# Kernel optimization log

Measured on AMD Instinct MI355X. Metric: run time of the kernel, lower is better.

## Reference

```python
import jax, jax.numpy as jnp
import numpy as np

PI = np.pi
EPS_A = 1e-4


def _frft_1d(x, a):
    """Chirp-z shear FRFT along the last axis. x: complex (..., N), a: scalar order."""
    a = jnp.clip(a, EPS_A, 2.0 - EPS_A)
    N = x.shape[-1]
    x = jnp.fft.ifftshift(x, axes=-1)
    alpha = a * PI / 2.0
    tan_a2 = jnp.tan(a * PI / 4.0)
    sin_a = jnp.sin(alpha)
    n = (jnp.arange(N, dtype=jnp.float32) - (N // 2))  # [-N/2, N/2)
    c1 = jnp.exp(-1j * PI * (n ** 2) * tan_a2 / N)      # chirp (depends on a)
    c2 = jnp.exp(-1j * PI * (n ** 2) / (N * sin_a))     # kernel chirp
    y = jnp.fft.ifft(jnp.fft.fft(x * c1, axis=-1) * c2, axis=-1)
    y = y * c1 / jnp.sqrt(jnp.abs(sin_a) + 1e-12)
    return jnp.fft.fftshift(y, axes=-1)


def _frft2d(x, ax, ay):
    # width pass (last axis) with ay, then height pass with ax -- same math as the
    # per-row / per-column torch loops, fully batched.
    y = _frft_1d(x, ay)                                   # over W
    y = jnp.swapaxes(_frft_1d(jnp.swapaxes(y, -1, -2), ax), -1, -2)  # over H
    return y


def setup_inputs() -> dict:
    key = jax.random.key(0)
    kx, = jax.random.split(key, 1)
    B, C, H, W = 4, 32, 256, 256
    x = jax.random.normal(kx, (B, C, H, W), dtype=jnp.float32)
    alpha = jnp.float32(0.5)
    # 1x1 conv weight (C, 2C): module init = copy of magnitude channels
    w = jnp.zeros((C, 2 * C), dtype=jnp.float32)
    w = w.at[jnp.arange(C), jnp.arange(C)].set(1.0)
    return {"x": x, "alpha": alpha, "w": w}


def reference(x, alpha, w):
    Xc = x.astype(jnp.complex64)
    Y = _frft2d(Xc, alpha, alpha)                        # (B, C, H, W) complex
    out = jnp.concatenate([jnp.abs(Y), jnp.angle(Y) / PI], axis=1)  # (B, 2C, H, W)
    out = jnp.einsum('oc,bchw->bohw', w, out)            # 1x1 conv, no bias
    return out.astype(x.dtype)
```

## Files before the change

kernel.cpp:

```cpp
#include <hip/hip_runtime.h>
#include <math.h>

#define B_N 4
#define C_N 32
#define H_N 256
#define W_N 256
#define PI_D 3.14159265358979323846
#define LSQ 257
#define LDW 260

typedef _Float16 half8 __attribute__((ext_vector_type(8)));
typedef float f32x4 __attribute__((ext_vector_type(4)));

__device__ __forceinline__ float2 cmul(float2 a, float2 b) {
    return make_float2(a.x * b.x - a.y * b.y, a.x * b.y + a.y * b.x);
}
__device__ __forceinline__ float2 f2add(float2 a, float2 b) {
    return make_float2(a.x + b.x, a.y + b.y);
}
__device__ __forceinline__ float2 f2sub(float2 a, float2 b) {
    return make_float2(a.x - b.x, a.y - b.y);
}

__device__ __forceinline__ void make_tables(int tid, const float* __restrict__ alpha_p,
                                            float2* c1l, float2* c2l, float2* twl,
                                            float* sscl) {
    if (tid < 256) {
        int j = tid;
        double a = fmin(fmax((double)alpha_p[0], 1e-4), 2.0 - 1e-4);
        double tan_a2 = tan(a * PI_D / 4.0);
        double sin_a  = sin(a * PI_D / 2.0);
        double n = (double)(j - 128);
        float sn, cs;

        double u1 = n * n * tan_a2 * (1.0 / 256.0);
        u1 -= 2.0 * floor(u1 * 0.5);
        __sincosf((float)(-PI_D * u1), &sn, &cs);
        c1l[j] = make_float2(cs, sn);

        double u2 = n * n / (256.0 * sin_a);
        u2 -= 2.0 * floor(u2 * 0.5);
        __sincosf((float)(-PI_D * u2), &sn, &cs);
        c2l[j] = make_float2(cs, sn);

        int k1 = j >> 4, t = j & 15;
        __sincosf((float)(-2.0 * PI_D * (double)(t * k1) * (1.0 / 256.0)), &sn, &cs);
        twl[j] = make_float2(cs, sn);

        if (j == 0) *sscl = (float)(1.0 / sqrt(fabs(sin_a) + 1e-12));
    }
}

template <bool INV>
__device__ __forceinline__ void fft16(float2* v) {
    const float C1 = 0.9238795325112867f, S1 = 0.3826834323650898f;
    const float C2 = 0.7071067811865476f;
    const float2 tw1 = make_float2(C1, INV ? S1 : -S1);
    const float2 tw2 = make_float2(C2, INV ? C2 : -C2);
    const float2 tw3 = make_float2(S1, INV ? C1 : -C1);
    const float2 tw4 = make_float2(0.0f, INV ? 1.0f : -1.0f);
    const float2 tw6 = make_float2(-C2, INV ? C2 : -C2);
    const float2 tw9 = make_float2(-C1, INV ? -S1 : S1);
    float2 u[16];
    #pragma unroll
    for (int n2 = 0; n2 < 4; ++n2) {
        float2 e0 = v[n2], e1 = v[4 + n2], e2 = v[8 + n2], e3 = v[12 + n2];
        float2 t0 = f2add(e0, e2), t1 = f2sub(e0, e2);
        float2 t2 = f2add(e1, e3), t3 = f2sub(e1, e3);
        float2 A0 = f2add(t0, t2);
        float2 A2 = f2sub(t0, t2);
        float2 A1, A3;
        if (!INV) { A1 = make_float2(t1.x + t3.y, t1.y - t3.x);
                    A3 = make_float2(t1.x - t3.y, t1.y + t3.x); }
        else      { A1 = make_float2(t1.x - t3.y, t1.y + t3.x);
                    A3 = make_float2(t1.x + t3.y, t1.y - t3.x); }
        u[n2] = A0;
        if (n2 == 0) { u[4 + n2] = A1;            u[8 + n2] = A2;            u[12 + n2] = A3; }
        if (n2 == 1) { u[4 + n2] = cmul(A1, tw1); u[8 + n2] = cmul(A2, tw2); u[12 + n2] = cmul(A3, tw3); }
        if (n2 == 2) { u[4 + n2] = cmul(A1, tw2); u[8 + n2] = cmul(A2, tw4); u[12 + n2] = cmul(A3, tw6); }
        if (n2 == 3) { u[4 + n2] = cmul(A1, tw3); u[8 + n2] = cmul(A2, tw6); u[12 + n2] = cmul(A3, tw9); }
    }
    #pragma unroll
    for (int k1 = 0; k1 < 4; ++k1) {
        float2 e0 = u[4 * k1], e1 = u[4 * k1 + 1], e2 = u[4 * k1 + 2], e3 = u[4 * k1 + 3];
        float2 t0 = f2add(e0, e2), t1 = f2sub(e0, e2);
        float2 t2 = f2add(e1, e3), t3 = f2sub(e1, e3);
        v[4 * k1 + 0] = f2add(t0, t2);
        v[4 * k1 + 2] = f2sub(t0, t2);
        if (!INV) { v[4 * k1 + 1] = make_float2(t1.x + t3.y, t1.y - t3.x);
                    v[4 * k1 + 3] = make_float2(t1.x - t3.y, t1.y + t3.x); }
        else      { v[4 * k1 + 1] = make_float2(t1.x - t3.y, t1.y + t3.x);
                    v[4 * k1 + 3] = make_float2(t1.x + t3.y, t1.y - t3.x); }
    }
}
#define REG(k) (4 * ((k) & 3) + ((k) >> 2))

__device__ __forceinline__ void frft_core16(float2* v, float2* __restrict__ sp,
                                            int t,
                                            const float2* __restrict__ c2l,
                                            const float2* __restrict__ twl) {
    fft16<false>(v);
    float2 w[16];
    #pragma unroll
    for (int k1 = 0; k1 < 16; ++k1)
        w[k1] = cmul(v[REG(k1)], twl[16 * k1 + t]);
    #pragma unroll
    for (int k1 = 0; k1 < 16; ++k1)
        sp[16 * k1 + (t ^ k1)] = w[k1];
    __syncthreads();
    #pragma unroll
    for (int n2 = 0; n2 < 16; ++n2)
        v[n2] = sp[16 * t + (n2 ^ t)];
    fft16<false>(v);
    #pragma unroll
    for (int k2 = 0; k2 < 16; ++k2)
        w[k2] = cmul(v[REG(k2)], c2l[t + 16 * k2]);
    fft16<true>(w);
    __syncthreads();
    #pragma unroll
    for (int m2 = 0; m2 < 16; ++m2) {
        float2 tw = twl[16 * m2 + t];
        tw.y = -tw.y;
        sp[16 * m2 + (t ^ m2)] = cmul(w[REG(m2)], tw);
    }
    __syncthreads();
    #pragma unroll
    for (int k1 = 0; k1 < 16; ++k1)
        v[k1] = sp[16 * t + (k1 ^ t)];
    fft16<true>(v);
}

__global__ __launch_bounds__(512, 4) void frft_cols_real(
        const float* __restrict__ x,
        const float* __restrict__ alpha_p,
        float2* __restrict__ Y) {
    __shared__ float2 s[32 * LSQ];
    __shared__ float2 c1l[256], c2l[256], twl[256];
    __shared__ float sscl;
    int tid = threadIdx.x;

    int blk = blockIdx.x;
    int w0 = (blk & 7) << 5;
    long long bc = blk >> 3;
    const float* xb = x + (bc << 16) + w0;

    float4 xv[4];
    #pragma unroll
    for (int p = 0; p < 4; ++p) {
        int idx = tid + (p << 9);
        int row = idx >> 3, c4 = idx & 7;
        xv[p] = *(const float4*)(xb + row * W_N + (c4 << 2));
    }

    make_tables(tid, alpha_p, c1l, c2l, twl, &sscl);

    float* fs = (float*)s;
    #pragma unroll
    for (int p = 0; p < 4; ++p) {
        int idx = tid + (p << 9);
        int row = idx >> 3, c4 = idx & 7;
        fs[(4 * c4 + 0) * (2 * LSQ) + row] = xv[p].x;
        fs[(4 * c4 + 1) * (2 * LSQ) + row] = xv[p].y;
        fs[(4 * c4 + 2) * (2 * LSQ) + row] = xv[p].z;
        fs[(4 * c4 + 3) * (2 * LSQ) + row] = xv[p].w;
    }
    __syncthreads();

    int seq = tid & 31, t = tid >> 5;
    float xs[16];
    #pragma unroll
    for (int n1 = 0; n1 < 16; ++n1)
        xs[n1] = fs[seq * (2 * LSQ) + 16 * (n1 ^ 8) + t];
    float scl_v = sscl;
    __syncthreads();

    float2 v[16];
    #pragma unroll
    for (int n1 = 0; n1 < 16; ++n1) {
        float2 c = c1l[16 * n1 + t];
        v[n1] = make_float2(xs[n1] * c.x, xs[n1] * c.y);
    }

    frft_core16(v, s + seq * LSQ, t, c2l, twl);

    float sc = scl_v * (1.0f / 256.0f);
    float2* Yb = Y + (bc << 16) + w0 + seq;
    #pragma unroll
    for (int m1 = 0; m1 < 16; ++m1) {
        float2 o = cmul(v[REG(m1)], c1l[16 * m1 + t]);
        Yb[(16 * (m1 ^ 8) + t) * W_N] = make_float2(o.x * sc, o.y * sc);
    }
}

__device__ __forceinline__ float fast_atan2(float y, float x) {
    float ax = fabsf(x), ay = fabsf(y);
    float mx = fmaxf(ax, ay), mn = fminf(ax, ay);
    float z = mn * __builtin_amdgcn_rcpf(fmaxf(mx, 1e-37f));
    float z2 = z * z;
    float p = fmaf(z2, -0.01172120f, 0.05265332f);
    p = fmaf(z2, p, -0.11643287f);
    p = fmaf(z2, p, 0.19354346f);
    p = fmaf(z2, p, -0.33262347f);
    p = fmaf(z2, p, 0.99997726f);
    p = p * z;
    float r = (ay > ax) ? (1.5707963f - p) : p;
    r = (x < 0.0f) ? (3.14159265f - r) : r;
    return copysignf(r, y);
}

__global__ __launch_bounds__(512, 4) void frft_rows_conv(
        const float2* __restrict__ Y,
        const float* __restrict__ alpha_p,
        const float* __restrict__ wmat, float* __restrict__ out) {
    __shared__ float2 s[32 * LSQ];
    __shared__ float2 c1l[256], c2l[256], twl[256];
    __shared__ float sscl;
    int tid = threadIdx.x;
    int t = tid & 15, ch = tid >> 4;

    int b = blockIdx.x >> 8, h = blockIdx.x & 255;
    const float2* xr = Y + (((long long)(b * C_N + ch)) << 16) + (h << 8);

    float2 v[16];
    #pragma unroll
    for (int n1 = 0; n1 < 16; ++n1)
        v[n1] = xr[16 * (n1 ^ 8) + t];

    make_tables(tid, alpha_p, c1l, c2l, twl, &sscl);
    __syncthreads();

    #pragma unroll
    for (int n1 = 0; n1 < 16; ++n1)
        v[n1] = cmul(v[n1], c1l[16 * n1 + t]);

    float2* sp = s + ch * LSQ;
    frft_core16(v, sp, t, c2l, twl);

    float sc = sscl * (1.0f / 256.0f);
    #pragma unroll
    for (int m1 = 0; m1 < 16; ++m1) {
        float2 o = cmul(v[REG(m1)], c1l[16 * m1 + t]);
        float mg = sc * sqrtf(fmaf(o.x, o.x, o.y * o.y));
        float an = fast_atan2(o.y, o.x) * 0.31830988618f;
        sp[16 * (m1 ^ 8) + t] = make_float2(mg, an);
    }
    __syncthreads();

    int lane = tid & 63, wv = tid >> 6;
    int q = lane >> 4, l15 = lane & 15;

    half8 bf[2][2];
    #pragma unroll
    for (int nt = 0; nt < 2; ++nt)
        #pragma unroll
        for (int kt = 0; kt < 2; ++kt) {
            const float* wp = wmat + (nt * 16 + l15) * 64 + kt * 32 + q * 8;
            float4 wa = *(const float4*)wp;
            float4 wb = *(const float4*)(wp + 4);
            bf[nt][kt][0] = (_Float16)wa.x; bf[nt][kt][1] = (_Float16)wa.y;
            bf[nt][kt][2] = (_Float16)wa.z; bf[nt][kt][3] = (_Float16)wa.w;
            bf[nt][kt][4] = (_Float16)wb.x; bf[nt][kt][5] = (_Float16)wb.y;
            bf[nt][kt][6] = (_Float16)wb.z; bf[nt][kt][7] = (_Float16)wb.w;
        }

    f32x4 acc[2][2];
    #pragma unroll
    for (int i = 0; i < 2; ++i)
        #pragma unroll
        for (int j = 0; j < 2; ++j)
            acc[i][j] = (f32x4){0.0f, 0.0f, 0.0f, 0.0f};

    #pragma unroll
    for (int mt2 = 0; mt2 < 2; ++mt2) {
        int mt = wv * 2 + mt2;
        int w = mt * 16 + l15;
        half8 am, aa;
        #pragma unroll
        for (int j = 0; j < 8; ++j) {
            float2 fv = s[(q * 8 + j) * LSQ + w];
            am[j] = (_Float16)fv.x;
            aa[j] = (_Float16)fv.y;
        }
        #pragma unroll
        for (int nt = 0; nt < 2; ++nt) {
            acc[mt2][nt] = __builtin_amdgcn_mfma_f32_16x16x32_f16(am, bf[nt][0], acc[mt2][nt], 0, 0, 0);
            acc[mt2][nt] = __builtin_amdgcn_mfma_f32_16x16x32_f16(aa, bf[nt][1], acc[mt2][nt], 0, 0, 0);
        }
    }
    __syncthreads();

    float* Ob = (float*)s;
    #pragma unroll
    for (int mt2 = 0; mt2 < 2; ++mt2) {
        int mt = wv * 2 + mt2;
        #pragma unroll
        for (int nt = 0; nt < 2; ++nt) {
            int o = nt * 16 + l15;
            *(f32x4*)&Ob[o * LDW + mt * 16 + q * 4] = acc[mt2][nt];
        }
    }
    __syncthreads();

    int o2 = tid >> 4, i16 = tid & 15;
    float* ob = out + (((long long)(b * C_N + o2)) << 16) + (h << 8);
    #pragma unroll
    for (int p = 0; p < 4; ++p) {
        int w4 = i16 * 4 + (p << 6);
        f32x4 val = *(f32x4*)&Ob[o2 * LDW + w4];
        *(f32x4*)(ob + w4) = val;
    }
}

extern "C" void kernel_launch(void* const* d_in, const int* in_sizes, int n_in,
                              void* d_out, int out_size, void* d_ws, size_t ws_size,
                              hipStream_t stream) {
    const float* x     = (const float*)d_in[0];
    const float* alpha = (const float*)d_in[1];
    const float* wmat  = (const float*)d_in[2];
    float* out = (float*)d_out;

    float2* Y = (float2*)d_ws;

    frft_cols_real<<<B_N * C_N * (W_N / 32), 512, 0, stream>>>(x, alpha, Y);

    frft_rows_conv<<<B_N * H_N, 512, 0, stream>>>(Y, alpha, wmat, out);
}
```

Baseline: 128.6 us.

## Make FFTs wave-local, stage column output in LDS, replace MFMA conv with FMA

The thread-to-sequence mapping in the column kernel becomes 16 threads per sequence, so each FFT lives inside one wavefront and the block-wide barriers in the FFT core become wave barriers. The column kernel now stages its output through LDS and writes Y as coalesced 16-byte rows instead of strided float2 stores. The row kernel's MFMA half-precision 1x1 conv, with its LDS transpose, is replaced by a per-thread fp32 FMA loop that reads weights with uniform scalar loads, and the launch-bounds occupancy hints are dropped. The conv now runs in fp32 on vector ALUs rather than matrix cores, and the weight reads and output stores are laid out differently.

```diff
diff --git a/kernel.cpp b/kernel.cpp
--- a/kernel.cpp
+++ b/kernel.cpp
@@ -7,9 +7,8 @@
 #define W_N 256
 #define PI_D 3.14159265358979323846
 #define LSQ 257
-#define LDW 260
-
-typedef _Float16 half8 __attribute__((ext_vector_type(8)));
+#define YROW 34
+
 typedef float f32x4 __attribute__((ext_vector_type(4)));
 
 __device__ __forceinline__ float2 cmul(float2 a, float2 b) {
@@ -107,7 +106,7 @@
     #pragma unroll
     for (int k1 = 0; k1 < 16; ++k1)
         sp[16 * k1 + (t ^ k1)] = w[k1];
-    __syncthreads();
+    __builtin_amdgcn_wave_barrier();
     #pragma unroll
     for (int n2 = 0; n2 < 16; ++n2)
         v[n2] = sp[16 * t + (n2 ^ t)];
@@ -116,25 +115,25 @@
     for (int k2 = 0; k2 < 16; ++k2)
         w[k2] = cmul(v[REG(k2)], c2l[t + 16 * k2]);
     fft16<true>(w);
-    __syncthreads();
+    __builtin_amdgcn_wave_barrier();
     #pragma unroll
     for (int m2 = 0; m2 < 16; ++m2) {
         float2 tw = twl[16 * m2 + t];
         tw.y = -tw.y;
         sp[16 * m2 + (t ^ m2)] = cmul(w[REG(m2)], tw);
     }
-    __syncthreads();
+    __builtin_amdgcn_wave_barrier();
     #pragma unroll
     for (int k1 = 0; k1 < 16; ++k1)
         v[k1] = sp[16 * t + (k1 ^ t)];
     fft16<true>(v);
 }
 
-__global__ __launch_bounds__(512, 4) void frft_cols_real(
+__global__ __launch_bounds__(512) void frft_cols_real(
         const float* __restrict__ x,
         const float* __restrict__ alpha_p,
         float2* __restrict__ Y) {
-    __shared__ float2 s[32 * LSQ];
+    __shared__ float2 s[H_N * YROW];
     __shared__ float2 c1l[256], c2l[256], twl[256];
     __shared__ float sscl;
     int tid = threadIdx.x;
@@ -166,13 +165,13 @@
     }
     __syncthreads();
 
-    int seq = tid & 31, t = tid >> 5;
+    int t = tid & 15, seq = tid >> 4;
     float xs[16];
     #pragma unroll
     for (int n1 = 0; n1 < 16; ++n1)
         xs[n1] = fs[seq * (2 * LSQ) + 16 * (n1 ^ 8) + t];
     float scl_v = sscl;
-    __syncthreads();
+    __builtin_amdgcn_wave_barrier();
 
     float2 v[16];
     #pragma unroll
@@ -184,11 +183,26 @@
     frft_core16(v, s + seq * LSQ, t, c2l, twl);
 
     float sc = scl_v * (1.0f / 256.0f);
-    float2* Yb = Y + (bc << 16) + w0 + seq;
+    float2 ov[16];
     #pragma unroll
     for (int m1 = 0; m1 < 16; ++m1) {
         float2 o = cmul(v[REG(m1)], c1l[16 * m1 + t]);
-        Yb[(16 * (m1 ^ 8) + t) * W_N] = make_float2(o.x * sc, o.y * sc);
+        ov[m1] = make_float2(o.x * sc, o.y * sc);
+    }
+    __syncthreads();
+
+    #pragma unroll
+    for (int m1 = 0; m1 < 16; ++m1)
+        s[(16 * (m1 ^ 8) + t) * YROW + seq] = ov[m1];
+    __syncthreads();
+
+    int seq2 = tid & 15, rr = tid >> 4;
+    float2* Yb = Y + (bc << 16) + w0;
+    #pragma unroll
+    for (int p = 0; p < 8; ++p) {
+        int row = rr + (p << 5);
+        f32x4 val = *(f32x4*)&s[row * YROW + 2 * seq2];
+        *(f32x4*)(Yb + (long long)row * W_N + 2 * seq2) = val;
     }
 }
 
@@ -208,7 +222,7 @@
     return copysignf(r, y);
 }
 
-__global__ __launch_bounds__(512, 4) void frft_rows_conv(
+__global__ __launch_bounds__(512) void frft_rows_conv(
         const float2* __restrict__ Y,
         const float* __restrict__ alpha_p,
         const float* __restrict__ wmat, float* __restrict__ out) {
@@ -237,6 +251,7 @@
     frft_core16(v, sp, t, c2l, twl);
 
     float sc = sscl * (1.0f / 256.0f);
+    __builtin_amdgcn_wave_barrier();
     #pragma unroll
     for (int m1 = 0; m1 < 16; ++m1) {
         float2 o = cmul(v[REG(m1)], c1l[16 * m1 + t]);
@@ -246,69 +261,28 @@
     }
     __syncthreads();
 
-    int lane = tid & 63, wv = tid >> 6;
-    int q = lane >> 4, l15 = lane & 15;
-
-    half8 bf[2][2];
-    #pragma unroll
-    for (int nt = 0; nt < 2; ++nt)
+    int w = tid & 255;
+    int obase = __builtin_amdgcn_readfirstlane((tid >> 8) << 4);
+    const float* wrow = wmat + obase * 64;
+
+    float acc[16];
+    #pragma unroll
+    for (int o = 0; o < 16; ++o) acc[o] = 0.0f;
+
+    #pragma unroll 4
+    for (int c = 0; c < C_N; ++c) {
+        float2 yv = s[c * LSQ + w];
         #pragma unroll
-        for (int kt = 0; kt < 2; ++kt) {
-            const float* wp = wmat + (nt * 16 + l15) * 64 + kt * 32 + q * 8;
-            float4 wa = *(const float4*)wp;
-            float4 wb = *(const float4*)(wp + 4);
-            bf[nt][kt][0] = (_Float16)wa.x; bf[nt][kt][1] = (_Float16)wa.y;
-            bf[nt][kt][2] = (_Float16)wa.z; bf[nt][kt][3] = (_Float16)wa.w;
-            bf[nt][kt][4] = (_Float16)wb.x; bf[nt][kt][5] = (_Float16)wb.y;
-            bf[nt][kt][6] = (_Float16)wb.z; bf[nt][kt][7] = (_Float16)wb.w;
+        for (int o = 0; o < 16; ++o) {
+            acc[o] = fmaf(wrow[o * 64 + c], yv.x, acc[o]);
+            acc[o] = fmaf(wrow[o * 64 + 32 + c], yv.y, acc[o]);
         }
-
-    f32x4 acc[2][2];
-    #pragma unroll
-    for (int i = 0; i < 2; ++i)
-        #pragma unroll
-        for (int j = 0; j < 2; ++j)
-            acc[i][j] = (f32x4){0.0f, 0.0f, 0.0f, 0.0f};
-
-    #pragma unroll
-    for (int mt2 = 0; mt2 < 2; ++mt2) {
-        int mt = wv * 2 + mt2;
-        int w = mt * 16 + l15;
-        half8 am, aa;
-        #pragma unroll
-        for (int j = 0; j < 8; ++j) {
-            float2 fv = s[(q * 8 + j) * LSQ + w];
-            am[j] = (_Float16)fv.x;
-            aa[j] = (_Float16)fv.y;
-        }
-        #pragma unroll
-        for (int nt = 0; nt < 2; ++nt) {
-            acc[mt2][nt] = __builtin_amdgcn_mfma_f32_16x16x32_f16(am, bf[nt][0], acc[mt2][nt], 0, 0, 0);
-            acc[mt2][nt] = __builtin_amdgcn_mfma_f32_16x16x32_f16(aa, bf[nt][1], acc[mt2][nt], 0, 0, 0);
-        }
-    }
-    __syncthreads();
-
-    float* Ob = (float*)s;
-    #pragma unroll
-    for (int mt2 = 0; mt2 < 2; ++mt2) {
-        int mt = wv * 2 + mt2;
-        #pragma unroll
-        for (int nt = 0; nt < 2; ++nt) {
-            int o = nt * 16 + l15;
-            *(f32x4*)&Ob[o * LDW + mt * 16 + q * 4] = acc[mt2][nt];
-        }
-    }
-    __syncthreads();
-
-    int o2 = tid >> 4, i16 = tid & 15;
-    float* ob = out + (((long long)(b * C_N + o2)) << 16) + (h << 8);
-    #pragma unroll
-    for (int p = 0; p < 4; ++p) {
-        int w4 = i16 * 4 + (p << 6);
-        f32x4 val = *(f32x4*)&Ob[o2 * LDW + w4];
-        *(f32x4*)(ob + w4) = val;
-    }
+    }
+
+    float* ob = out + (((long long)(b * C_N + obase)) << 16) + (h << 8) + w;
+    #pragma unroll
+    for (int o = 0; o < 16; ++o)
+        ob[(long long)o << 16] = acc[o];
 }
 
 extern "C" void kernel_launch(void* const* d_in, const int* in_sizes, int n_in,
```

After: 179.8 us. 1.4x slower.
